# Kernel optimization log

Measured on AMD Instinct MI355X. Metric: run time of the kernel, lower is better.

## Reference

```python
import jax, jax.numpy as jnp
import numpy as np

B, N, C = 4, 48 * 64, 256
H, W = 48, 64


def _positional_encodings(batch, dtype=jnp.float32):
    # (x^2, y^2, xy, x, y, 1) encoding; matches get_positional_encodings with intrinsics=None
    ys = jnp.linspace(-1.0, 1.0, H, dtype=dtype)
    xs = jnp.linspace(-1.0, 1.0, W, dtype=dtype)
    p3 = jnp.tile(ys, W)            # [N] : ys repeated W times (torch .repeat(B, w))
    p4 = jnp.repeat(xs, H)          # [N] : each x repeated H times (repeat_interleave)
    pos = jnp.stack([p3 * p3, p4 * p4, p3 * p4, p3, p4, jnp.ones_like(p3)], axis=-1)  # [N,6]
    return jnp.broadcast_to(pos, (batch, N, 6))


def setup_inputs() -> dict:
    key = jax.random.key(0)
    k1, k2, k3, k4 = jax.random.split(key, 4)
    x1 = jax.random.normal(k1, (B, N, C), dtype=jnp.float32)
    x2 = jax.random.normal(k2, (B, N, C), dtype=jnp.float32)
    corr = jax.random.normal(k3, (B, 1, H, W, H, W), dtype=jnp.float32)
    W_proj = jax.random.normal(k4, (C + 6, C), dtype=jnp.float32) * (1.0 / np.sqrt(C + 6))
    b_proj = jnp.zeros((C,), dtype=jnp.float32)
    return {"x1": x1, "x2": x2, "corr": corr, "W_proj": W_proj, "b_proj": b_proj}


def reference(x1, x2, corr, W_proj, b_proj):
    b, n, c = x1.shape
    a = corr.reshape(b, n, n)                      # squeeze(1) + double flatten
    # dual softmax (row-wise * column-wise)
    s_row = jax.nn.softmax(a, axis=-1)
    s_col = jax.nn.softmax(a, axis=-2)
    attn_f1 = s_row * s_col                        # [B,N,N]
    attn_f2 = jnp.swapaxes(attn_f1, -2, -1)        # softmax(a^T,-1)*softmax(a^T,-2) == attn_f1^T

    pos = _positional_encodings(b, dtype=x1.dtype)
    v1 = jnp.concatenate([x1, pos], axis=2)        # [B,N,C+6]
    v2 = jnp.concatenate([x2, pos], axis=2)

    # bilinear products v^T @ attn @ v  -> [B, C+6, C+6]
    fund1 = jnp.einsum('bnc,bnm,bmd->bcd', v1, attn_f1, v1)
    fund2 = jnp.einsum('bnc,bnm,bmd->bcd', v2, attn_f2, v2)

    fund1 = jnp.swapaxes(fund1, -2, -1)
    fund2 = jnp.swapaxes(fund2, -2, -1)

    out1 = fund1 @ W_proj + b_proj                 # proj_fundamental
    out2 = fund2 @ W_proj + b_proj
    return (out2, out1)                            # (fundamental_2, fundamental_1)
```

## Files before the change

### kernel.cpp

```cpp
#include <hip/hip_runtime.h>
#include <math.h>

#define NB 4
#define NN 3072
#define NC 256
#define CP 262
#define KG 384
#define XW 528
#define MD 272
#define K3S 4
#define HH 48
#define WW 64
#define LOG2E 1.4426950408889634f

typedef short short8 __attribute__((ext_vector_type(8)));
typedef short short4v __attribute__((ext_vector_type(4)));
typedef float f32x4 __attribute__((ext_vector_type(4)));
typedef unsigned int uint4v __attribute__((ext_vector_type(4)));

__device__ __forceinline__ float fexp2(float x) {
#if __has_builtin(__builtin_amdgcn_exp2f)
    return __builtin_amdgcn_exp2f(x);
#else
    return __exp2f(x);
#endif
}

__device__ __forceinline__ void bsplit(float v, short& h, short& l) {
    unsigned u = __float_as_uint(v);
    h = (short)(u >> 16);
    float r = v - __uint_as_float(u & 0xFFFF0000u);
    l = (short)(__float_as_uint(r) >> 16);
}

__device__ __forceinline__ void fma4(float4& c, float a, float4 b) {
    c.x = fmaf(a, b.x, c.x);
    c.y = fmaf(a, b.y, c.y);
    c.z = fmaf(a, b.z, c.z);
    c.w = fmaf(a, b.w, c.w);
}

__global__ __launch_bounds__(256) void k_stats(const float* __restrict__ corr,
                                               const float* __restrict__ x1,
                                               const float* __restrict__ x2,
                                               float* __restrict__ colpart,
                                               float* __restrict__ rlS,
                                               short* __restrict__ Xh, short* __restrict__ Xl) {
    int bid = blockIdx.x;
    int t = threadIdx.x;
    if (bid < 1024) {
        int chunk = bid & 255;
        int b = bid >> 8;
        int r0 = chunk * 12;
        const float* base = corr + ((size_t)b * NN + r0) * NN;
        f32x4 colacc[3];
        const f32x4 zz = {0.f, 0.f, 0.f, 0.f};
#pragma unroll
        for (int c = 0; c < 3; c++) colacc[c] = zz;
        float rowpart[12];
#pragma unroll 2
        for (int r = 0; r < 12; r++) {
            float rp = 0.f;
#pragma unroll
            for (int cp = 0; cp < 3; cp++) {
                f32x4 v = *(const f32x4*)(base + (size_t)r * NN + cp * 1024 + t * 4);
                f32x4 e;
                e[0] = __expf(v[0]); e[1] = __expf(v[1]);
                e[2] = __expf(v[2]); e[3] = __expf(v[3]);
                colacc[cp] += e;
                rp += (e[0] + e[1]) + (e[2] + e[3]);
            }
            rowpart[r] = rp;
        }
        __shared__ float red[4][12];
        int w = t >> 6, l = t & 63;
#pragma unroll
        for (int r = 0; r < 12; r++) {
            float rp = rowpart[r];
#pragma unroll
            for (int off = 1; off < 64; off <<= 1) rp += __shfl_xor(rp, off);
            if (l == 0) red[w][r] = rp;
        }
        __syncthreads();
        if (t < 12)
            rlS[b * NN + r0 + t] = __log2f(red[0][t] + red[1][t] + red[2][t] + red[3][t]);
        float* cp = colpart + (size_t)(b * 256 + chunk) * NN;
#pragma unroll
        for (int c = 0; c < 3; c++)
            *(f32x4*)(cp + c * 1024 + t * 4) = colacc[c];
    } else {
        int id = (bid - 1024) * 256 + t;
        int col = id % XW;
        int rest = id / XW;
        int kg = rest % KG;
        int b = rest / KG;
        short* ph = Xh + (size_t)id * 8;
        short* pl = Xl + (size_t)id * 8;
        if (col < 512) {
            const float* src = (col < 256 ? x1 : x2) + ((size_t)b * NN + kg * 8) * NC + (col & 255);
#pragma unroll
            for (int j = 0; j < 8; j++) {
                short hs, ls;
                bsplit(src[(size_t)j * NC], hs, ls);
                ph[j] = hs; pl[j] = ls;
            }
        } else {
            int c = col - 512;
#pragma unroll
            for (int j = 0; j < 8; j++) {
                int k = kg * 8 + j;
                int ip4 = k / HH;
                int ip3 = k - ip4 * HH;
                float p3 = -1.f + 2.f * (float)ip3 / 47.f;
                float p4 = -1.f + 2.f * (float)ip4 / 63.f;
                float v = 0.f;
                if (c == 0) v = p3 * p3;
                else if (c == 1) v = p4 * p4;
                else if (c == 2) v = p3 * p4;
                else if (c == 3) v = p3;
                else if (c == 4) v = p4;
                else if (c == 5) v = 1.f;
                short hs, ls;
                bsplit(v, hs, ls);
                ph[j] = hs; pl[j] = ls;
            }
        }
    }
}

__global__ __launch_bounds__(256) void k_comb(const float* __restrict__ colpart,
                                              float* __restrict__ ccS) {
    int idx = blockIdx.x * 256 + threadIdx.x;
    int b = idx / NN;
    int m = idx - b * NN;
    const float* cp = colpart + (size_t)b * 256 * NN + m;
    float s0 = 0.f, s1 = 0.f, s2 = 0.f, s3 = 0.f;
    for (int ch = 0; ch < 256; ch += 4) {
        s0 += cp[(size_t)(ch + 0) * NN];
        s1 += cp[(size_t)(ch + 1) * NN];
        s2 += cp[(size_t)(ch + 2) * NN];
        s3 += cp[(size_t)(ch + 3) * NN];
    }
    ccS[idx] = __log2f((s0 + s1) + (s2 + s3));
}

struct SMemMain {
    unsigned AH[2][48 * 32];
    unsigned AL[2][48 * 32];
    float ccsh[NN];
};
union SMemU {
    SMemMain m;
    float pdump[2 * 64 * 12];
};

#define LOAD_B4(PH, PL, BHF, BLF)                                            \
    {                                                                        \
        _Pragma("unroll") for (int i_ = 0; i_ < 4; i_++) {                   \
            BHF[i_] = *(const short8*)((PH) + i_ * 128);                     \
            BLF[i_] = *(const short8*)((PL) + i_ * 128);                     \
        }                                                                    \
    }

#define READ_AFRAGS3(BUFH, BUFL, UNIT, AHF, ALF)                             \
    {                                                                        \
        _Pragma("unroll") for (int fr_ = 0; fr_ < 3; fr_++) {                \
            int rowr_ = fr_ * 16 + row16;                                    \
            int uidx_ = rowr_ * 32 + (((UNIT) ^ (rowr_ & 7)) << 2);          \
            AHF[fr_] = *(const short8*)&(BUFH)[uidx_];                       \
            ALF[fr_] = *(const short8*)&(BUFL)[uidx_];                       \
        }                                                                    \
    }

#define MFMA_CLUSTER34(AHF, ALF, BHF, BLF)                                                         \
    {                                                                                              \
        _Pragma("unroll") for (int fr_ = 0; fr_ < 3; fr_++)                                        \
        _Pragma("unroll") for (int i_ = 0; i_ < 4; i_++)                                           \
            acc[fr_][i_] = __builtin_amdgcn_mfma_f32_16x16x32_bf16(AHF[fr_], BHF[i_], acc[fr_][i_], 0, 0, 0); \
        _Pragma("unroll") for (int fr_ = 0; fr_ < 3; fr_++)                                        \
        _Pragma("unroll") for (int i_ = 0; i_ < 4; i_++)                                           \
            acc[fr_][i_] = __builtin_amdgcn_mfma_f32_16x16x32_bf16(AHF[fr_], BLF[i_], acc[fr_][i_], 0, 0, 0); \
        _Pragma("unroll") for (int fr_ = 0; fr_ < 3; fr_++)                                        \
        _Pragma("unroll") for (int i_ = 0; i_ < 4; i_++)                                           \
            acc[fr_][i_] = __builtin_amdgcn_mfma_f32_16x16x32_bf16(ALF[fr_], BHF[i_], acc[fr_][i_], 0, 0, 0); \
    }

#define POS_CLUSTER3(AHF, ALF, PBH, PBL)                                                           \
    {                                                                                              \
        _Pragma("unroll") for (int fr_ = 0; fr_ < 3; fr_++) {                                      \
            accP[fr_] = __builtin_amdgcn_mfma_f32_16x16x32_bf16(AHF[fr_], (PBH), accP[fr_], 0, 0, 0); \
            accP[fr_] = __builtin_amdgcn_mfma_f32_16x16x32_bf16(AHF[fr_], (PBL), accP[fr_], 0, 0, 0); \
            accP[fr_] = __builtin_amdgcn_mfma_f32_16x16x32_bf16(ALF[fr_], (PBH), accP[fr_], 0, 0, 0); \
        }                                                                                          \
    }

#define STAGE_A8(DSTH, DSTL, PC)                                                                  \
    {                                                                                             \
        f32x4 ccv0 = *(const f32x4*)&ccsh[(PC) * 64 + g * 8];                                     \
        f32x4 ccv1 = *(const f32x4*)&ccsh[(PC) * 64 + g * 8 + 4];                                 \
        float ev[8];                                                                              \
        _Pragma("unroll") for (int q_ = 0; q_ < 4; q_++) {                                        \
            ev[q_]     = fexp2(fmaf(C2, cr0[q_], rmn) - ccv0[q_]);                                \
            ev[4 + q_] = fexp2(fmaf(C2, cr1[q_], rmn) - ccv1[q_]);                                \
        }                                                                                         \
        uint4v hi, lo;                                                                            \
        _Pragma("unroll") for (int q_ = 0; q_ < 4; q_++) {                                        \
            unsigned u0 = __float_as_uint(ev[2 * q_]);                                            \
            unsigned u1 = __float_as_uint(ev[2 * q_ + 1]);                                        \
            hi[q_] = __builtin_amdgcn_perm(u1, u0, 0x07060302u);                                  \
            float r0_ = ev[2 * q_] - __uint_as_float(u0 & 0xffff0000u);                           \
            float r1_ = ev[2 * q_ + 1] - __uint_as_float(u1 & 0xffff0000u);                       \
            lo[q_] = __builtin_amdgcn_perm(__float_as_uint(r1_), __float_as_uint(r0_), 0x07060302u); \
        }                                                                                         \
        *(uint4v*)&(DSTH)[widx] = hi;                                                             \
        *(uint4v*)&(DSTL)[widx] = lo;                                                             \
    }

__global__ __launch_bounds__(512, 2) void k2_mfma(const float* __restrict__ corr,
        const short* __restrict__ Xh, const short* __restrict__ Xl,
        const float* __restrict__ rlS, const float* __restrict__ ccS,
        short* __restrict__ Zh, short* __restrict__ Zl) {
    __shared__ SMemU sm;
    float* ccsh = sm.m.ccsh;

    const float C2 = 2.f * LOG2E;
    const size_t BSTEP = (size_t)4 * XW * 8;

    int bid = blockIdx.x;
    int xcd = bid & 7, sub = bid >> 3;
    int b = xcd >> 1;
    int rowblk = (xcd & 1) + (sub << 1);
    int n0 = rowblk * 48;

    int t = threadIdx.x;
    int w = t >> 6, l = t & 63;
    int row16 = l & 15, slot = l >> 4;
    bool duty6 = (w == 6);
    bool duty7 = (w == 7);
    bool writer = (t < 384);
    int wrow = t >> 3, g = t & 7;
    int widx = wrow * 32 + ((g ^ (wrow & 7)) << 2);

    {
        const f32x4* src = (const f32x4*)(ccS + (size_t)b * NN);
        for (int i = t; i < NN / 4; i += 512) ((f32x4*)ccsh)[i] = src[i];
    }

    const float* corrR = corr;
    float rmn = 0.f;
    if (writer) {
        corrR = corr + ((size_t)b * NN + n0 + wrow) * NN + g * 8;
        rmn = -rlS[b * NN + n0 + wrow];
    }

    int col0 = w * 64 + row16;
    const short* bh = Xh + ((size_t)(b * KG + slot) * XW + col0) * 8;
    const short* bl = Xl + ((size_t)(b * KG + slot) * XW + col0) * 8;

    f32x4 acc[3][4];
    f32x4 accP[3];
    const f32x4 zz = {0.f, 0.f, 0.f, 0.f};
#pragma unroll
    for (int fr = 0; fr < 3; fr++) {
#pragma unroll
        for (int i = 0; i < 4; i++) acc[fr][i] = zz;
        accP[fr] = zz;
    }

    short8 BhA[4], BlA[4], BhB[4], BlB[4];
    short8 P0h = {0,0,0,0,0,0,0,0}, P0l = P0h, P1h = P0h, P1l = P0h;
    LOAD_B4(bh, bl, BhA, BlA);

    f32x4 cr0, cr1;
    __syncthreads();
    if (writer) {
        cr0 = *(const f32x4*)(corrR);
        cr1 = *(const f32x4*)(corrR + 4);
        STAGE_A8(sm.m.AH[0], sm.m.AL[0], 0);
        cr0 = *(const f32x4*)(corrR + 64);
        cr1 = *(const f32x4*)(corrR + 68);
    }
    asm volatile("s_waitcnt lgkmcnt(0)" ::: "memory");
    __builtin_amdgcn_s_barrier();

    int cur = 0;
    for (int p = 0; p < 48; ++p) {
        const unsigned* AHc = &sm.m.AH[cur][0];
        const unsigned* ALc = &sm.m.AL[cur][0];
        unsigned* AHn = &sm.m.AH[cur ^ 1][0];
        unsigned* ALn = &sm.m.AL[cur ^ 1][0];
        short8 Ah[3], Al[3];
        READ_AFRAGS3(AHc, ALc, slot, Ah, Al);
        bh += BSTEP; bl += BSTEP;
        LOAD_B4(bh, bl, BhB, BlB);
        if (duty6) {
            size_t o0 = ((size_t)(b * KG + p * 8 + slot) * XW + 512 + row16) * 8;
            P0h = *(const short8*)(Xh + o0);
            P0l = *(const short8*)(Xl + o0);
        }
        __builtin_amdgcn_s_setprio(1);
        MFMA_CLUSTER34(Ah, Al, BhA, BlA);
        if (duty6) POS_CLUSTER3(Ah, Al, P0h, P0l);
        __builtin_amdgcn_s_setprio(0);
        READ_AFRAGS3(AHc, ALc, 4 + slot, Ah, Al);
        if (p < 47) {
            bh += BSTEP; bl += BSTEP;
            LOAD_B4(bh, bl, BhA, BlA);
        }
        if (duty7) {
            size_t o1 = ((size_t)(b * KG + p * 8 + 4 + slot) * XW + 512 + row16) * 8;
            P1h = *(const short8*)(Xh + o1);
            P1l = *(const short8*)(Xl + o1);
        }
        if (writer) {
            int pc = (p + 1 < 48) ? p + 1 : 47;
            STAGE_A8(AHn, ALn, pc);
            int pn = (p + 2 < 48) ? p + 2 : 47;
            cr0 = *(const f32x4*)(corrR + pn * 64);
            cr1 = *(const f32x4*)(corrR + pn * 64 + 4);
        }
        __builtin_amdgcn_s_setprio(1);
        MFMA_CLUSTER34(Ah, Al, BhB, BlB);
        if (duty7) POS_CLUSTER3(Ah, Al, P1h, P1l);
        __builtin_amdgcn_s_setprio(0);
        asm volatile("s_waitcnt lgkmcnt(0)" ::: "memory");
        __builtin_amdgcn_s_barrier();
        cur ^= 1;
    }

#pragma unroll
    for (int fr = 0; fr < 3; fr++) {
        int kgz = rowblk * 6 + fr * 2 + (slot >> 1);
        int jb = (slot & 1) << 2;
#pragma unroll
        for (int i = 0; i < 4; i++) {
            int colv = w * 64 + i * 16 + row16;
            size_t off = ((size_t)(b * KG + kgz) * XW + colv) * 8 + jb;
            short4v zh, zl;
#pragma unroll
            for (int r = 0; r < 4; r++) {
                short hs, ls; bsplit(acc[fr][i][r], hs, ls);
                zh[r] = hs; zl[r] = ls;
            }
            *(short4v*)(Zh + off) = zh;
            *(short4v*)(Zl + off) = zl;
        }
    }
    if (w >= 6) {
#pragma unroll
        for (int fr = 0; fr < 3; fr++)
            *(f32x4*)&sm.pdump[(size_t)((w - 6) * 64 + l) * 12 + fr * 4] = accP[fr];
    }
    __syncthreads();
    if (t < 192) {
        int fr = t >> 6, ll = t & 63;
        int sl = ll >> 4, r16 = ll & 15;
        f32x4 s = *(const f32x4*)&sm.pdump[(size_t)ll * 12 + fr * 4]
                + *(const f32x4*)&sm.pdump[(size_t)(64 + ll) * 12 + fr * 4];
        int kgz = rowblk * 6 + fr * 2 + (sl >> 1);
        int jb = (sl & 1) << 2;
        size_t off = ((size_t)(b * KG + kgz) * XW + 512 + r16) * 8 + jb;
        short4v zh, zl;
#pragma unroll
        for (int r = 0; r < 4; r++) {
            short hs, ls; bsplit(s[r], hs, ls);
            zh[r] = hs; zl[r] = ls;
        }
        *(short4v*)(Zh + off) = zh;
        *(short4v*)(Zl + off) = zl;
    }
}

__global__ __launch_bounds__(256) void k3_mfma(const short* __restrict__ Xh, const short* __restrict__ Xl,
                                               const short* __restrict__ Zh, const short* __restrict__ Zl,
                                               float* __restrict__ Mpart) {
    int tile = blockIdx.x;
    int rt = tile / 3, ct = tile % 3;
    int mb = blockIdx.y;
    int mat = mb >> 2, b = mb & 3;
    int split = blockIdx.z;

    const int O0[4] = {0, 6, 12, 17};
    int r0f = O0[rt], rNf = O0[rt + 1] - r0f;
    int c0f = O0[ct], cNf = O0[ct + 1] - c0f;

    int t = threadIdx.x;
    int w = t >> 6, l = t & 63;
    int row16 = l & 15, slot = l >> 4;
    int wr = w >> 1, wc = w & 1;
    int rh = (rNf + 1) >> 1;
    int rbeg = r0f + (wr ? rh : 0);
    int rcnt = wr ? (rNf - rh) : rh;
    int chh = (cNf + 1) >> 1;
    int cbeg = c0f + (wc ? chh : 0);
    int ccnt = wc ? (cNf - chh) : chh;

    const short *Ah_, *Al_, *Bh_, *Bl_;
    int abase, bbase;
    if (mat == 0) { Ah_ = Xh; Al_ = Xl; Bh_ = Zh; Bl_ = Zl; abase = 0; bbase = 0; }
    else          { Ah_ = Zh; Al_ = Zl; Bh_ = Xh; Bl_ = Xl; abase = 256; bbase = 256; }

    int acol[3], bcol[3];
#pragma unroll
    for (int i = 0; i < 3; i++) {
        int fa = rbeg + i;
        acol[i] = ((fa < 16) ? (abase + fa * 16) : 512) + row16;
        int fb = cbeg + i;
        bcol[i] = ((fb < 16) ? (bbase + fb * 16) : 512) + row16;
    }

    f32x4 acc[3][3];
    const f32x4 zz = {0.f, 0.f, 0.f, 0.f};
#pragma unroll
    for (int i = 0; i < 3; i++)
#pragma unroll
        for (int j = 0; j < 3; j++) acc[i][j] = zz;

    for (int it = 0; it < 24; it++) {
        int kg = split * 96 + it * 4 + slot;
        size_t base = (size_t)(b * KG + kg) * XW;
        short8 Ah[3], Al[3], Bhf[3], Blf[3];
#pragma unroll
        for (int i = 0; i < 3; i++) {
            if (i < rcnt) {
                Ah[i] = *(const short8*)(Ah_ + (base + acol[i]) * 8);
                Al[i] = *(const short8*)(Al_ + (base + acol[i]) * 8);
            }
            if (i < ccnt) {
                Bhf[i] = *(const short8*)(Bh_ + (base + bcol[i]) * 8);
                Blf[i] = *(const short8*)(Bl_ + (base + bcol[i]) * 8);
            }
        }
#pragma unroll
        for (int i = 0; i < 3; i++) {
            if (i < rcnt) {
#pragma unroll
                for (int j = 0; j < 3; j++) {
                    if (j < ccnt) {
                        acc[i][j] = __builtin_amdgcn_mfma_f32_16x16x32_bf16(Ah[i], Bhf[j], acc[i][j], 0, 0, 0);
                        acc[i][j] = __builtin_amdgcn_mfma_f32_16x16x32_bf16(Al[i], Bhf[j], acc[i][j], 0, 0, 0);
                        acc[i][j] = __builtin_amdgcn_mfma_f32_16x16x32_bf16(Ah[i], Blf[j], acc[i][j], 0, 0, 0);
                    }
                }
            }
        }
    }

    float* Mp = Mpart + (size_t)(mb * K3S + split) * (MD * MD);
#pragma unroll
    for (int i = 0; i < 3; i++) {
        if (i < rcnt) {
#pragma unroll
            for (int j = 0; j < 3; j++) {
                if (j < ccnt) {
                    int r = (rbeg + i) * 16 + slot * 4;
                    int c = (cbeg + j) * 16 + row16;
#pragma unroll
                    for (int q = 0; q < 4; q++)
                        Mp[(size_t)(r + q) * MD + c] = acc[i][j][q];
                }
            }
        }
    }
}

__global__ __launch_bounds__(256) void k_mcombine(const float* __restrict__ Mpart, float* __restrict__ M) {
    const int per = MD * MD;
    int f4 = blockIdx.x * 256 + threadIdx.x;
    if (f4 >= (8 * per) / 4) return;
    int e = f4 * 4;
    int mb = e / per;
    int off = e - mb * per;
    const float* src = Mpart + (size_t)mb * K3S * per + off;
    float4 s = make_float4(0.f, 0.f, 0.f, 0.f);
#pragma unroll
    for (int sp = 0; sp < K3S; sp++) {
        float4 v = *(const float4*)(src + (size_t)sp * per);
        s.x += v.x; s.y += v.y; s.z += v.z; s.w += v.w;
    }
    *(float4*)(M + (size_t)mb * per + off) = s;
}

__global__ __launch_bounds__(256) void k4_proj(const float* __restrict__ M, const float* __restrict__ Wp,
                                               const float* __restrict__ bp, float* __restrict__ out) {
    int i0 = blockIdx.x * 16;
    int b = blockIdx.y;
    int mat = blockIdx.z;
    const float* Mp = M + (size_t)(mat * 4 + b) * (MD * MD);
    int t = threadIdx.x;
    int jt = t & 63, it = t >> 6;
    int j = jt * 4;
    float4 a0 = make_float4(0.f, 0.f, 0.f, 0.f), a1 = a0, a2 = a0, a3 = a0;
#pragma unroll 2
    for (int k = 0; k < CP; k++) {
        float4 w = *(const float4*)(Wp + (size_t)k * NC + j);
        float4 g = *(const float4*)(Mp + (size_t)k * MD + i0 + it * 4);
        fma4(a0, g.x, w); fma4(a1, g.y, w); fma4(a2, g.z, w); fma4(a3, g.w, w);
    }
    float4 bb = *(const float4*)(bp + j);
    a0.x += bb.x; a0.y += bb.y; a0.z += bb.z; a0.w += bb.w;
    a1.x += bb.x; a1.y += bb.y; a1.z += bb.z; a1.w += bb.w;
    a2.x += bb.x; a2.y += bb.y; a2.z += bb.z; a2.w += bb.w;
    a3.x += bb.x; a3.y += bb.y; a3.z += bb.z; a3.w += bb.w;
    float* ob = out + (mat == 0 ? (size_t)NB * CP * NC : (size_t)0) + (size_t)b * CP * NC;
    int i = i0 + it * 4;
    if (i + 0 < CP) *(float4*)(ob + (size_t)(i + 0) * NC + j) = a0;
    if (i + 1 < CP) *(float4*)(ob + (size_t)(i + 1) * NC + j) = a1;
    if (i + 2 < CP) *(float4*)(ob + (size_t)(i + 2) * NC + j) = a2;
    if (i + 3 < CP) *(float4*)(ob + (size_t)(i + 3) * NC + j) = a3;
}

extern "C" void kernel_launch(void* const* d_in, const int* in_sizes, int n_in,
                              void* d_out, int out_size, void* d_ws, size_t ws_size,
                              hipStream_t stream) {
    const float* x1 = (const float*)d_in[0];
    const float* x2 = (const float*)d_in[1];
    const float* corr = (const float*)d_in[2];
    const float* Wp = (const float*)d_in[3];
    const float* bp = (const float*)d_in[4];
    float* out = (float*)d_out;
    float* w = (float*)d_ws;

    const size_t XSZ = (size_t)NB * KG * XW * 8;

    size_t o = 0;
    float* rlS = w + o;     o += NB * NN;
    float* ccS = w + o;     o += NB * NN;
    float* colpart = w + o; o += (size_t)NB * 256 * NN;
    short* Xh = (short*)(w + o); o += XSZ / 2;
    short* Xl = (short*)(w + o); o += XSZ / 2;
    short* Zh = (short*)(w + o); o += XSZ / 2;
    short* Zl = (short*)(w + o); o += XSZ / 2;
    float* Mpart = w + o; o += (size_t)8 * K3S * MD * MD;
    float* M = w + o;     o += (size_t)8 * MD * MD;

    k_stats<<<dim3(4192), dim3(256), 0, stream>>>(corr, x1, x2, colpart, rlS, Xh, Xl);
    k_comb<<<dim3(48), dim3(256), 0, stream>>>(colpart, ccS);
    k2_mfma<<<dim3(256), dim3(512), 0, stream>>>(corr, Xh, Xl, rlS, ccS, Zh, Zl);
    k3_mfma<<<dim3(9, 8, K3S), dim3(256), 0, stream>>>(Xh, Xl, Zh, Zl, Mpart);
    k_mcombine<<<dim3(578), dim3(256), 0, stream>>>(Mpart, M);
    k4_proj<<<dim3(17, NB, 2), dim3(256), 0, stream>>>(M, Wp, bp, out);
}
```

Baseline: 257.8 us.

## Double k2 stage depth to 128 columns per barrier and parallelize column-sum combine

The main k2 loop now stages 128 columns of exp-weighted attention per shared-memory buffer instead of 64. That halves the barrier count to 24 iterations, each with four MFMA clusters, and spreads the positional-encoding MFMA work across four waves instead of two. The k_comb reduction is split across four thread groups with a shared-memory combine, and runs on 192 blocks instead of 48 to expose more parallelism. Costs are doubled LDS for the A buffers, more registers for the extra corr loads, and possible occupancy pressure at two blocks per CU.

```diff
diff --git a/kernel.cpp b/kernel.cpp
--- a/kernel.cpp
+++ b/kernel.cpp
@@ -130,28 +130,35 @@
 
 __global__ __launch_bounds__(256) void k_comb(const float* __restrict__ colpart,
                                               float* __restrict__ ccS) {
-    int idx = blockIdx.x * 256 + threadIdx.x;
-    int b = idx / NN;
-    int m = idx - b * NN;
+    int bid = blockIdx.x;
+    int b = bid / 48, cg = bid - (bid / 48) * 48;
+    int t = threadIdx.x;
+    int q = t >> 6, c = t & 63;
+    int m = cg * 64 + c;
     const float* cp = colpart + (size_t)b * 256 * NN + m;
     float s0 = 0.f, s1 = 0.f, s2 = 0.f, s3 = 0.f;
-    for (int ch = 0; ch < 256; ch += 4) {
+    int ch0 = q * 64;
+    for (int ch = ch0; ch < ch0 + 64; ch += 4) {
         s0 += cp[(size_t)(ch + 0) * NN];
         s1 += cp[(size_t)(ch + 1) * NN];
         s2 += cp[(size_t)(ch + 2) * NN];
         s3 += cp[(size_t)(ch + 3) * NN];
     }
-    ccS[idx] = __log2f((s0 + s1) + (s2 + s3));
+    __shared__ float red[4][64];
+    red[q][c] = (s0 + s1) + (s2 + s3);
+    __syncthreads();
+    if (t < 64)
+        ccS[(size_t)b * NN + cg * 64 + t] = __log2f(red[0][t] + red[1][t] + red[2][t] + red[3][t]);
 }
 
 struct SMemMain {
-    unsigned AH[2][48 * 32];
-    unsigned AL[2][48 * 32];
+    unsigned AH[2][48 * 64];
+    unsigned AL[2][48 * 64];
     float ccsh[NN];
 };
 union SMemU {
     SMemMain m;
-    float pdump[2 * 64 * 12];
+    float pdump[4 * 64 * 12];
 };
 
 #define LOAD_B4(PH, PL, BHF, BLF)                                            \
@@ -166,7 +173,7 @@
     {                                                                        \
         _Pragma("unroll") for (int fr_ = 0; fr_ < 3; fr_++) {                \
             int rowr_ = fr_ * 16 + row16;                                    \
-            int uidx_ = rowr_ * 32 + (((UNIT) ^ (rowr_ & 7)) << 2);          \
+            int uidx_ = rowr_ * 64 + (((UNIT) ^ (rowr_ & 7)) << 2);          \
             AHF[fr_] = *(const short8*)&(BUFH)[uidx_];                       \
             ALF[fr_] = *(const short8*)&(BUFL)[uidx_];                       \
         }                                                                    \
@@ -194,26 +201,38 @@
         }                                                                                          \
     }
 
-#define STAGE_A8(DSTH, DSTL, PC)                                                                  \
+#define STAGE_A16(DSTH, DSTL, PC)                                                                 \
     {                                                                                             \
-        f32x4 ccv0 = *(const f32x4*)&ccsh[(PC) * 64 + g * 8];                                     \
-        f32x4 ccv1 = *(const f32x4*)&ccsh[(PC) * 64 + g * 8 + 4];                                 \
-        float ev[8];                                                                              \
+        f32x4 ccv0 = *(const f32x4*)&ccsh[(PC) * 128 + g * 8];                                    \
+        f32x4 ccv1 = *(const f32x4*)&ccsh[(PC) * 128 + g * 8 + 4];                                \
+        f32x4 ccv2 = *(const f32x4*)&ccsh[(PC) * 128 + 64 + g * 8];                               \
+        f32x4 ccv3 = *(const f32x4*)&ccsh[(PC) * 128 + 64 + g * 8 + 4];                           \
+        float ev[16];                                                                             \
         _Pragma("unroll") for (int q_ = 0; q_ < 4; q_++) {                                        \
-            ev[q_]     = fexp2(fmaf(C2, cr0[q_], rmn) - ccv0[q_]);                                \
-            ev[4 + q_] = fexp2(fmaf(C2, cr1[q_], rmn) - ccv1[q_]);                                \
+            ev[q_]      = fexp2(fmaf(C2, cr0[q_], rmn) - ccv0[q_]);                               \
+            ev[4 + q_]  = fexp2(fmaf(C2, cr1[q_], rmn) - ccv1[q_]);                               \
+            ev[8 + q_]  = fexp2(fmaf(C2, cr2[q_], rmn) - ccv2[q_]);                               \
+            ev[12 + q_] = fexp2(fmaf(C2, cr3[q_], rmn) - ccv3[q_]);                               \
         }                                                                                         \
-        uint4v hi, lo;                                                                            \
+        uint4v hi0, hi1, lo0, lo1;                                                                \
         _Pragma("unroll") for (int q_ = 0; q_ < 4; q_++) {                                        \
             unsigned u0 = __float_as_uint(ev[2 * q_]);                                            \
             unsigned u1 = __float_as_uint(ev[2 * q_ + 1]);                                        \
-            hi[q_] = __builtin_amdgcn_perm(u1, u0, 0x07060302u);                                  \
+            hi0[q_] = __builtin_amdgcn_perm(u1, u0, 0x07060302u);                                 \
             float r0_ = ev[2 * q_] - __uint_as_float(u0 & 0xffff0000u);                           \
             float r1_ = ev[2 * q_ + 1] - __uint_as_float(u1 & 0xffff0000u);                       \
-            lo[q_] = __builtin_amdgcn_perm(__float_as_uint(r1_), __float_as_uint(r0_), 0x07060302u); \
+            lo0[q_] = __builtin_amdgcn_perm(__float_as_uint(r1_), __float_as_uint(r0_), 0x07060302u); \
+            unsigned v0 = __float_as_uint(ev[8 + 2 * q_]);                                        \
+            unsigned v1 = __float_as_uint(ev[8 + 2 * q_ + 1]);                                    \
+            hi1[q_] = __builtin_amdgcn_perm(v1, v0, 0x07060302u);                                 \
+            float t0_ = ev[8 + 2 * q_] - __uint_as_float(v0 & 0xffff0000u);                       \
+            float t1_ = ev[8 + 2 * q_ + 1] - __uint_as_float(v1 & 0xffff0000u);                   \
+            lo1[q_] = __builtin_amdgcn_perm(__float_as_uint(t1_), __float_as_uint(t0_), 0x07060302u); \
         }                                                                                         \
-        *(uint4v*)&(DSTH)[widx] = hi;                                                             \
-        *(uint4v*)&(DSTL)[widx] = lo;                                                             \
+        *(uint4v*)&(DSTH)[widx0] = hi0;                                                           \
+        *(uint4v*)&(DSTH)[widx1] = hi1;                                                           \
+        *(uint4v*)&(DSTL)[widx0] = lo0;                                                           \
+        *(uint4v*)&(DSTL)[widx1] = lo1;                                                           \
     }
 
 __global__ __launch_bounds__(512, 2) void k2_mfma(const float* __restrict__ corr,
@@ -235,11 +254,10 @@
     int t = threadIdx.x;
     int w = t >> 6, l = t & 63;
     int row16 = l & 15, slot = l >> 4;
-    bool duty6 = (w == 6);
-    bool duty7 = (w == 7);
     bool writer = (t < 384);
     int wrow = t >> 3, g = t & 7;
-    int widx = wrow * 32 + ((g ^ (wrow & 7)) << 2);
+    int widx0 = wrow * 64 + ((g ^ (wrow & 7)) << 2);
+    int widx1 = widx0 + 32;
 
     {
         const f32x4* src = (const f32x4*)(ccS + (size_t)b * NN);
@@ -268,60 +286,77 @@
     }
 
     short8 BhA[4], BlA[4], BhB[4], BlB[4];
-    short8 P0h = {0,0,0,0,0,0,0,0}, P0l = P0h, P1h = P0h, P1l = P0h;
+    short8 Ph = {0,0,0,0,0,0,0,0}, Pl = Ph;
     LOAD_B4(bh, bl, BhA, BlA);
 
-    f32x4 cr0, cr1;
+    f32x4 cr0, cr1, cr2, cr3;
     __syncthreads();
     if (writer) {
         cr0 = *(const f32x4*)(corrR);
         cr1 = *(const f32x4*)(corrR + 4);
-        STAGE_A8(sm.m.AH[0], sm.m.AL[0], 0);
-        cr0 = *(const f32x4*)(corrR + 64);
-        cr1 = *(const f32x4*)(corrR + 68);
+        cr2 = *(const f32x4*)(corrR + 64);
+        cr3 = *(const f32x4*)(corrR + 68);
+        STAGE_A16(sm.m.AH[0], sm.m.AL[0], 0);
+        cr0 = *(const f32x4*)(corrR + 128);
+        cr1 = *(const f32x4*)(corrR + 132);
+        cr2 = *(const f32x4*)(corrR + 192);
+        cr3 = *(const f32x4*)(corrR + 196);
     }
     asm volatile("s_waitcnt lgkmcnt(0)" ::: "memory");
     __builtin_amdgcn_s_barrier();
 
     int cur = 0;
-    for (int p = 0; p < 48; ++p) {
+    for (int sp = 0; sp < 24; ++sp) {
         const unsigned* AHc = &sm.m.AH[cur][0];
         const unsigned* ALc = &sm.m.AL[cur][0];
         unsigned* AHn = &sm.m.AH[cur ^ 1][0];
         unsigned* ALn = &sm.m.AL[cur ^ 1][0];
         short8 Ah[3], Al[3];
+        if (w < 4) {
+            size_t o0 = ((size_t)(b * KG + sp * 16 + 4 * w + slot) * XW + 512 + row16) * 8;
+            Ph = *(const short8*)(Xh + o0);
+            Pl = *(const short8*)(Xl + o0);
+        }
         READ_AFRAGS3(AHc, ALc, slot, Ah, Al);
         bh += BSTEP; bl += BSTEP;
         LOAD_B4(bh, bl, BhB, BlB);
-        if (duty6) {
-            size_t o0 = ((size_t)(b * KG + p * 8 + slot) * XW + 512 + row16) * 8;
-            P0h = *(const short8*)(Xh + o0);
-            P0l = *(const short8*)(Xl + o0);
-        }
         __builtin_amdgcn_s_setprio(1);
         MFMA_CLUSTER34(Ah, Al, BhA, BlA);
-        if (duty6) POS_CLUSTER3(Ah, Al, P0h, P0l);
+        if (w == 0) POS_CLUSTER3(Ah, Al, Ph, Pl);
         __builtin_amdgcn_s_setprio(0);
         READ_AFRAGS3(AHc, ALc, 4 + slot, Ah, Al);
-        if (p < 47) {
+        bh += BSTEP; bl += BSTEP;
+        LOAD_B4(bh, bl, BhA, BlA);
+        __builtin_amdgcn_s_setprio(1);
+        MFMA_CLUSTER34(Ah, Al, BhB, BlB);
+        if (w == 1) POS_CLUSTER3(Ah, Al, Ph, Pl);
+        __builtin_amdgcn_s_setprio(0);
+        if (writer) {
+            int pc = (sp + 1 < 24) ? sp + 1 : 23;
+            STAGE_A16(AHn, ALn, pc);
+        }
+        READ_AFRAGS3(AHc, ALc, 8 + slot, Ah, Al);
+        bh += BSTEP; bl += BSTEP;
+        LOAD_B4(bh, bl, BhB, BlB);
+        __builtin_amdgcn_s_setprio(1);
+        MFMA_CLUSTER34(Ah, Al, BhA, BlA);
+        if (w == 2) POS_CLUSTER3(Ah, Al, Ph, Pl);
+        __builtin_amdgcn_s_setprio(0);
+        if (writer) {
+            int pn = (sp + 2 < 24) ? sp + 2 : 23;
+            cr0 = *(const f32x4*)(corrR + pn * 128);
+            cr1 = *(const f32x4*)(corrR + pn * 128 + 4);
+            cr2 = *(const f32x4*)(corrR + pn * 128 + 64);
+            cr3 = *(const f32x4*)(corrR + pn * 128 + 68);
+        }
+        READ_AFRAGS3(AHc, ALc, 12 + slot, Ah, Al);
+        if (sp < 23) {
             bh += BSTEP; bl += BSTEP;
             LOAD_B4(bh, bl, BhA, BlA);
         }
-        if (duty7) {
-            size_t o1 = ((size_t)(b * KG + p * 8 + 4 + slot) * XW + 512 + row16) * 8;
-            P1h = *(const short8*)(Xh + o1);
-            P1l = *(const short8*)(Xl + o1);
-        }
-        if (writer) {
-            int pc = (p + 1 < 48) ? p + 1 : 47;
-            STAGE_A8(AHn, ALn, pc);
-            int pn = (p + 2 < 48) ? p + 2 : 47;
-            cr0 = *(const f32x4*)(corrR + pn * 64);
-            cr1 = *(const f32x4*)(corrR + pn * 64 + 4);
-        }
         __builtin_amdgcn_s_setprio(1);
         MFMA_CLUSTER34(Ah, Al, BhB, BlB);
-        if (duty7) POS_CLUSTER3(Ah, Al, P1h, P1l);
+        if (w == 3) POS_CLUSTER3(Ah, Al, Ph, Pl);
         __builtin_amdgcn_s_setprio(0);
         asm volatile("s_waitcnt lgkmcnt(0)" ::: "memory");
         __builtin_amdgcn_s_barrier();
@@ -346,17 +381,19 @@
             *(short4v*)(Zl + off) = zl;
         }
     }
-    if (w >= 6) {
+    if (w < 4) {
 #pragma unroll
         for (int fr = 0; fr < 3; fr++)
-            *(f32x4*)&sm.pdump[(size_t)((w - 6) * 64 + l) * 12 + fr * 4] = accP[fr];
+            *(f32x4*)&sm.pdump[(size_t)(w * 64 + l) * 12 + fr * 4] = accP[fr];
     }
     __syncthreads();
     if (t < 192) {
         int fr = t >> 6, ll = t & 63;
         int sl = ll >> 4, r16 = ll & 15;
-        f32x4 s = *(const f32x4*)&sm.pdump[(size_t)ll * 12 + fr * 4]
-                + *(const f32x4*)&sm.pdump[(size_t)(64 + ll) * 12 + fr * 4];
+        f32x4 s = zz;
+#pragma unroll
+        for (int ww = 0; ww < 4; ww++)
+            s += *(const f32x4*)&sm.pdump[(size_t)(ww * 64 + ll) * 12 + fr * 4];
         int kgz = rowblk * 6 + fr * 2 + (sl >> 1);
         int jb = (sl & 1) << 2;
         size_t off = ((size_t)(b * KG + kgz) * XW + 512 + r16) * 8 + jb;
@@ -535,7 +572,7 @@
     float* M = w + o;     o += (size_t)8 * MD * MD;
 
     k_stats<<<dim3(4192), dim3(256), 0, stream>>>(corr, x1, x2, colpart, rlS, Xh, Xl);
-    k_comb<<<dim3(48), dim3(256), 0, stream>>>(colpart, ccS);
+    k_comb<<<dim3(192), dim3(256), 0, stream>>>(colpart, ccS);
     k2_mfma<<<dim3(256), dim3(512), 0, stream>>>(corr, Xh, Xl, rlS, ccS, Zh, Zl);
     k3_mfma<<<dim3(9, 8, K3S), dim3(256), 0, stream>>>(Xh, Xl, Zh, Zl, Mpart);
     k_mcombine<<<dim3(578), dim3(256), 0, stream>>>(Mpart, M);
```

Measured after the change: 267.4 us. +3.7%, slower.
